# Kernel optimization log

Hardware: AMD Instinct MI355X
Metric: run time of the kernel (lower is better)

Reference implementation:

```python
import jax, jax.numpy as jnp
from jax import lax
import numpy as np

B, C, H, W = 4, 256, 64, 64
O, KH, KW = 256, 3, 3
STR, PAD, DIL = 1, 1, 1
K = KH * KW
EPS = 1e-5


def setup_inputs() -> dict:
    key = jax.random.key(0)
    ks = jax.random.split(key, 8)
    fan = 1.0 / np.sqrt(C * KH * KW)
    return {
        "input_x": jax.random.normal(ks[0], (B, C, H, W), jnp.float32),
        # offset-generating conv (DeformConv2dPack style): 2*K channels of (dy, dx)
        "w_offset": jax.random.normal(ks[1], (2 * K, C, KH, KW), jnp.float32) * 0.01,
        "b_offset": jnp.zeros((2 * K,), jnp.float32),
        # deformable conv weight / bias
        "weight": jax.random.normal(ks[2], (O, C, KH, KW), jnp.float32) * fan,
        "bias": jax.random.normal(ks[3], (O,), jnp.float32) * 0.01,
        # BatchNorm2d params + running stats (inference mode)
        "gamma": jax.random.normal(ks[4], (O,), jnp.float32) * 0.1 + 1.0,
        "beta": jax.random.normal(ks[5], (O,), jnp.float32) * 0.1,
        "run_mean": jax.random.normal(ks[6], (O,), jnp.float32) * 0.1,
        "run_var": jax.random.uniform(ks[7], (O,), jnp.float32, 0.5, 1.5),
    }


def _bilinear_sample(img, y, x):
    """img: [B,C,H,W]; y,x: [B,K,Ho,Wo] float sample coords. Zero outside."""
    y0 = jnp.floor(y)
    x0 = jnp.floor(x)
    ly = y - y0
    lx = x - x0
    y0i = y0.astype(jnp.int32)
    x0i = x0.astype(jnp.int32)
    y1i = y0i + 1
    x1i = x0i + 1

    def valid(yi, xi):
        return ((yi >= 0) & (yi < H) & (xi >= 0) & (xi < W)).astype(img.dtype)

    # per-corner interpolation weights, zeroed when the corner is out of bounds
    w00 = (1 - ly) * (1 - lx) * valid(y0i, x0i)
    w01 = (1 - ly) * lx * valid(y0i, x1i)
    w10 = ly * (1 - lx) * valid(y1i, x0i)
    w11 = ly * lx * valid(y1i, x1i)

    y0c = jnp.clip(y0i, 0, H - 1)
    y1c = jnp.clip(y1i, 0, H - 1)
    x0c = jnp.clip(x0i, 0, W - 1)
    x1c = jnp.clip(x1i, 0, W - 1)

    gather = jax.vmap(lambda im, yi, xi: im[:, yi, xi])  # -> [B,C,K,Ho,Wo]
    out = gather(img, y0c, x0c) * w00[:, None]
    out = out + gather(img, y0c, x1c) * w01[:, None]
    out = out + gather(img, y1c, x0c) * w10[:, None]
    out = out + gather(img, y1c, x1c) * w11[:, None]
    return out  # [B,C,K,Ho,Wo]


def reference(input_x, w_offset, b_offset, weight, bias, gamma, beta, run_mean, run_var):
    # 1) generate offsets with a regular conv (DeformConv2dPack conv_offset)
    offset = lax.conv_general_dilated(
        input_x, w_offset, (STR, STR), [(PAD, PAD), (PAD, PAD)],
        rhs_dilation=(DIL, DIL), dimension_numbers=("NCHW", "OIHW", "NCHW"))
    offset = offset + b_offset[None, :, None, None]  # [B, 2K, Ho, Wo]
    Ho, Wo = offset.shape[2], offset.shape[3]
    off = offset.reshape(B, K, 2, Ho, Wo)
    dy, dx = off[:, :, 0], off[:, :, 1]  # [B,K,Ho,Wo]

    # 2) base sampling grid for each kernel tap
    ky, kx = jnp.meshgrid(jnp.arange(KH), jnp.arange(KW), indexing="ij")
    base_y = (jnp.arange(Ho) * STR - PAD)[None, :, None] + (ky.reshape(-1) * DIL)[:, None, None]
    base_x = (jnp.arange(Wo) * STR - PAD)[None, None, :] + (kx.reshape(-1) * DIL)[:, None, None]
    y = base_y.astype(input_x.dtype) + dy  # [B,K,Ho,Wo]
    x = base_x.astype(input_x.dtype) + dx

    # 3) bilinear-sampled im2col then dense contraction
    sampled = _bilinear_sample(input_x, y, x)  # [B,C,K,Ho,Wo]
    out = jnp.einsum("bckhw,ock->bohw", sampled, weight.reshape(O, C, K))
    out = out + bias[None, :, None, None]

    # 4) BatchNorm (inference, running stats) + ReLU
    inv = gamma / jnp.sqrt(run_var + EPS)
    out = out * inv[None, :, None, None] + (beta - run_mean * inv)[None, :, None, None]
    return jax.nn.relu(out)
```

## Files before the change

kernel.cpp:

```cpp
#include <hip/hip_runtime.h>
#include <math.h>

typedef __attribute__((ext_vector_type(8))) short b8;
typedef __attribute__((ext_vector_type(4))) float f4;
typedef float f4u __attribute__((ext_vector_type(4), aligned(4)));
typedef _Float16 h8 __attribute__((ext_vector_type(8)));
typedef _Float16 h2 __attribute__((ext_vector_type(2)));

#define XT2   0
#define OF2   2097152
#define DW2   2392064
#define DP2   2981888
#define AF2   3571712
#define BF2   3866624
#define WH2   2392064
#define WL2   2428928

__device__ inline ushort f2bf(float f) {
  uint u = __float_as_uint(f);
  return (ushort)((u + 0x7FFFu + ((u >> 16) & 1u)) >> 16);
}
__device__ inline h2 u2h2(uint u) { union { uint u; h2 h; } x; x.u = u; return x.h; }
__device__ inline uint h22u(h2 h) { union { uint u; h2 h; } x; x.h = h; return x.u; }
__device__ inline uint duph(float f) {
  union { _Float16 h; ushort u; } x; x.h = (_Float16)f;
  return ((uint)x.u << 16) | x.u;
}

__global__ __launch_bounds__(256) void prep_k(
    const float* __restrict__ w, const float* __restrict__ wof,
    const float* __restrict__ bias,
    const float* __restrict__ gamma, const float* __restrict__ beta,
    const float* __restrict__ mean, const float* __restrict__ var,
    float* __restrict__ ws) {
  const int tid = blockIdx.x * 256 + threadIdx.x;
  const int l  = tid & 63;
  const int ot = (tid >> 6) & 15;
  const int f  = tid >> 10;
  const int o  = (ot << 4) + (l & 15);
  const float inv = gamma[o] * rsqrtf(var[o] + 1e-5f);
  {
    const int s  = f & 1;
    const int g  = f >> 1;
    const int cw = g / 9;
    const int kk = g - cw * 9;
    const int cb = (cw << 6) + (s << 5) + ((l >> 4) << 3);
    h8 pk;
#pragma unroll
    for (int j = 0; j < 8; ++j)
      pk[j] = (_Float16)(w[((o << 8) + cb + j) * 9 + kk] * inv);
    *(h8*)((_Float16*)(ws + AF2) + tid * 8) = pk;
    ((f4*)(ws + OF2))[tid] = f4{0.f, 0.f, 0.f, 0.f};
  }
  if (tid < 256) {
    const float iv = gamma[tid] * rsqrtf(var[tid] + 1e-5f);
    ws[BF2 + tid] = bias[tid] * iv + beta[tid] - mean[tid] * iv;
  }
  if (tid < 9216) {
    const int l2  = tid & 63;
    const int mt  = (tid >> 6) & 1;
    const int i2  = tid >> 7;
    const int cg2 = i2 / 9;
    const int kk2 = i2 - cg2 * 9;
    const int oc  = (mt << 4) + (l2 & 15);
    const int cb2 = (cg2 << 5) + ((l2 >> 4) << 3);
    b8 ph, pl;
#pragma unroll
    for (int j = 0; j < 8; ++j) {
      const float v = (oc < 18) ? wof[((oc << 8) + cb2 + j) * 9 + kk2] : 0.f;
      const ushort h = f2bf(v);
      const float hf = __uint_as_float((uint)h << 16);
      ph[j] = (short)h;
      pl[j] = (short)f2bf(v - hf);
    }
    *(b8*)((short*)(ws + WH2) + tid * 8) = ph;
    *(b8*)((short*)(ws + WL2) + tid * 8) = pl;
  }
}

__global__ __launch_bounds__(256) void transpose_k(
    const float* __restrict__ x, float* __restrict__ ws) {
  const int id  = blockIdx.x * 256 + threadIdx.x;
  const int p   = id & 4095;
  const int cg8 = (id >> 12) & 31;
  const int b   = id >> 17;
  const float* xp = x + (((long)(b * 256 + cg8 * 8)) << 12) + p;
  _Float16* xt = (_Float16*)(ws + XT2);
  h8 pk;
#pragma unroll
  for (int j = 0; j < 8; ++j) pk[j] = (_Float16)xp[(long)j << 12];
  *(h8*)(xt + ((((long)(b << 12) + p)) << 8) + (cg8 << 3)) = pk;
}

__global__ __launch_bounds__(256, 4) void offset_part_k(
    const float* __restrict__ x, float* __restrict__ ws) {
  __shared__ __align__(16) ushort Xh[3][66][40];
  __shared__ __align__(16) ushort Xl[3][66][40];
  const int bid = blockIdx.x;
  const int q   = bid >> 8;
  const int b   = (bid >> 6) & 3;
  const int ho  = bid & 63;
  const int t   = threadIdx.x;
  const int l   = t & 63;
  const int wv  = t >> 6;
  const short* afh = (const short*)(ws + WH2);
  const short* afl = (const short*)(ws + WL2);

  for (int u = t; u < 240; u += 256) {
    const int row = u / 80, rem = u % 80;
    const int col = (rem >= 40) ? 65 : 0;
    const int c   = rem % 40;
    Xh[row][col][c] = 0;
    Xl[row][col][c] = 0;
  }

  f4 acc[2];
  acc[0] = f4{0.f, 0.f, 0.f, 0.f};
  acc[1] = f4{0.f, 0.f, 0.f, 0.f};

  const int cidx = t >> 3;
  const int j8   = t & 7;
  const float* xc = x + ((long)b << 20) + ((long)cidx << 12);
  const int col = (wv << 4) + (l & 15);
  const int qc  = (l >> 4) << 3;

  for (int it = 0; it < 2; ++it) {
    const int cg = (q << 1) + it;
    __syncthreads();
    const float* xg = xc + ((long)(cg << 5) << 12);
#pragma unroll
    for (int rep = 0; rep < 6; ++rep) {
      const int fi   = (rep << 3) + j8;
      const int row  = fi >> 4;
      const int colf = (fi & 15) << 2;
      const int y = ho - 1 + row;
      f4u v = {0.f, 0.f, 0.f, 0.f};
      if (y >= 0 && y <= 63) v = *(const f4u*)(xg + (y << 6) + colf);
#pragma unroll
      for (int qq = 0; qq < 4; ++qq) {
        const ushort h = f2bf(v[qq]);
        const float hf = __uint_as_float((uint)h << 16);
        Xh[row][colf + 1 + qq][cidx] = h;
        Xl[row][colf + 1 + qq][cidx] = f2bf(v[qq] - hf);
      }
    }
    __syncthreads();
#pragma unroll
    for (int kk = 0; kk < 9; ++kk) {
      const int ky = kk / 3, kx = kk - ky * 3;
      const int i  = cg * 9 + kk;
      const b8 ah0 = *(const b8*)(afh + ((((i << 1) + 0) << 6) + l) * 8);
      const b8 ah1 = *(const b8*)(afh + ((((i << 1) + 1) << 6) + l) * 8);
      const b8 al0 = *(const b8*)(afl + ((((i << 1) + 0) << 6) + l) * 8);
      const b8 al1 = *(const b8*)(afl + ((((i << 1) + 1) << 6) + l) * 8);
      const b8 bh = *(const b8*)&Xh[ky][col + kx][qc];
      const b8 bl = *(const b8*)&Xl[ky][col + kx][qc];
      acc[0] = __builtin_amdgcn_mfma_f32_16x16x32_bf16(ah0, bh, acc[0], 0, 0, 0);
      acc[0] = __builtin_amdgcn_mfma_f32_16x16x32_bf16(ah0, bl, acc[0], 0, 0, 0);
      acc[0] = __builtin_amdgcn_mfma_f32_16x16x32_bf16(al0, bh, acc[0], 0, 0, 0);
      acc[1] = __builtin_amdgcn_mfma_f32_16x16x32_bf16(ah1, bh, acc[1], 0, 0, 0);
      acc[1] = __builtin_amdgcn_mfma_f32_16x16x32_bf16(ah1, bl, acc[1], 0, 0, 0);
      acc[1] = __builtin_amdgcn_mfma_f32_16x16x32_bf16(al1, bh, acc[1], 0, 0, 0);
    }
  }

  const int wo = col;
  const int q4 = (l >> 4) << 2;
#pragma unroll
  for (int mt = 0; mt < 2; ++mt)
#pragma unroll
    for (int r = 0; r < 4; ++r) {
      const int oc = (mt << 4) + q4 + r;
      if (oc < 18)
        atomicAdd(&ws[OF2 + ((b * 18 + oc) << 12) + (ho << 6) + wo],
                  acc[mt][r]);
    }
}

__global__ __launch_bounds__(256) void make_desc_xt(
    const float* __restrict__ bof, float* __restrict__ ws) {
  const int d  = blockIdx.x * 256 + threadIdx.x;
  const int k  = d >> 14;
  const int n  = d & 16383;
  const int b  = n >> 12;
  const int sp = n & 4095;
  const int ho = sp >> 6, wo = sp & 63;
  const int ky = k / 3, kx = k - ky * 3;
  const float dy = ws[OF2 + ((b * 18 + (k << 1)) << 12) + sp] + bof[k << 1];
  const float dx = ws[OF2 + ((b * 18 + (k << 1) + 1) << 12) + sp] + bof[(k << 1) + 1];
  const float py = (float)(ho - 1 + ky) + dy;
  const float px = (float)(wo - 1 + kx) + dx;
  const float y0f = floorf(py), x0f = floorf(px);
  const float ly = py - y0f, lx = px - x0f;
  const int y0 = (int)y0f, x0 = (int)x0f;
  const int y1 = y0 + 1, x1 = x0 + 1;
  const float vy0 = (y0 >= 0 && y0 < 64) ? 1.f : 0.f;
  const float vy1 = (y1 >= 0 && y1 < 64) ? 1.f : 0.f;
  const float vx0 = (x0 >= 0 && x0 < 64) ? 1.f : 0.f;
  const float vx1 = (x1 >= 0 && x1 < 64) ? 1.f : 0.f;
  const int y0c = min(max(y0, 0), 63), y1c = min(max(y1, 0), 63);
  const int x0c = min(max(x0, 0), 63), x1c = min(max(x1, 0), 63);
  uint4 wv;
  wv.x = duph((1.f - ly) * (1.f - lx) * vy0 * vx0);
  wv.y = duph((1.f - ly) * lx * vy0 * vx1);
  wv.z = duph(ly * (1.f - lx) * vy1 * vx0);
  wv.w = duph(ly * lx * vy1 * vx1);
  int4 pv;
  pv.x = (y0c << 6) + x0c;
  pv.y = (y0c << 6) + x1c;
  pv.z = (y1c << 6) + x0c;
  pv.w = (y1c << 6) + x1c;
  ((uint4*)(ws + DW2))[d] = wv;
  ((int4*)(ws + DP2))[d] = pv;
}

__global__ __launch_bounds__(256, 2) void deform_gemm_f16b(
    const float* __restrict__ ws, float* __restrict__ out) {
  __shared__ __align__(16) uint Bs[3][32][32];
  __shared__ uint4 dW[288];
  __shared__ int4  dP[288];

  const int t     = threadIdx.x;
  const int bid   = blockIdx.x;
  const int xcd   = bid & 7;
  const int batch = xcd >> 1;
  const int half  = xcd & 1;
  const int j     = bid >> 3;
  const int sp0   = (half << 11) + (j << 5);
  const int nd0   = (batch << 12) + sp0;
  const int l     = t & 63;
  const int wv    = t >> 6;

  const int sn  = ((wv & 1) << 4) | (l & 15);
  const int cg8 = ((wv >> 1) << 2) | (l >> 4);
  const uint* xtu = (const uint*)(ws + XT2) + ((long)batch << 19);
  const _Float16* af = (const _Float16*)(ws + AF2);

  for (int u = t; u < 288; u += 256) {
    const int kk = u >> 5, s = u & 31;
    const int dg = (kk << 14) + nd0 + s;
    dW[u] = ((const uint4*)(ws + DW2))[dg];
    dP[u] = ((const int4*)(ws + DP2))[dg];
  }
  __syncthreads();

  f4 acc[4][2];
#pragma unroll
  for (int m = 0; m < 4; ++m)
#pragma unroll
    for (int nt = 0; nt < 2; ++nt) acc[m][nt] = f4{0.f, 0.f, 0.f, 0.f};

  uint4 cset0[4], cset1[4];
  uint4 w0v, w1v, wq; int4 pq;
  h8 aA[4][2], aN[4][2];
  int kkd, kkg, cwg, bufc;

#define FRDD(W_, P_, KK_) do { const int u_ = ((KK_) << 5) + sn;             \
    W_ = dW[u_]; P_ = dP[u_]; } while (0)

#define FGATH(DST_, P_) do {                                                 \
    const int co_ = (cwg << 5) + (cg8 << 2);                                 \
    DST_[0] = *(const uint4*)(xtu + ((P_).x << 7) + co_);                    \
    DST_[1] = *(const uint4*)(xtu + ((P_).y << 7) + co_);                    \
    DST_[2] = *(const uint4*)(xtu + ((P_).z << 7) + co_);                    \
    DST_[3] = *(const uint4*)(xtu + ((P_).w << 7) + co_);                    \
  } while (0)

#define FCOMB(CS_, WV_, BUF_) do {                                           \
    const h2 wc0_ = u2h2((WV_).x), wc1_ = u2h2((WV_).y);                     \
    const h2 wc2_ = u2h2((WV_).z), wc3_ = u2h2((WV_).w);                     \
    uint4 r_;                                                                \
    r_.x = h22u(u2h2(CS_[0].x) * wc0_ + u2h2(CS_[1].x) * wc1_ +              \
                u2h2(CS_[2].x) * wc2_ + u2h2(CS_[3].x) * wc3_);              \
    r_.y = h22u(u2h2(CS_[0].y) * wc0_ + u2h2(CS_[1].y) * wc1_ +              \
                u2h2(CS_[2].y) * wc2_ + u2h2(CS_[3].y) * wc3_);              \
    r_.z = h22u(u2h2(CS_[0].z) * wc0_ + u2h2(CS_[1].z) * wc1_ +              \
                u2h2(CS_[2].z) * wc2_ + u2h2(CS_[3].z) * wc3_);              \
    r_.w = h22u(u2h2(CS_[0].w) * wc0_ + u2h2(CS_[1].w) * wc1_ +              \
                u2h2(CS_[2].w) * wc2_ + u2h2(CS_[3].w) * wc3_);              \
    *(uint4*)&Bs[BUF_][sn][(cg8 ^ (sn & 7)) << 2] = r_;                      \
  } while (0)

#define FLOADA(I_, DST_) do {                                                \
    _Pragma("unroll")                                                        \
    for (int m = 0; m < 4; ++m)                                              \
      _Pragma("unroll")                                                      \
      for (int s = 0; s < 2; ++s) {                                          \
        const int f_ = ((I_) << 1) + s;                                      \
        DST_[m][s] = *(const h8*)(af +                                       \
            ((((f_ << 4) + (wv << 2) + m) << 6) + l) * 8);                   \
      }                                                                      \
  } while (0)

#define FMFMA(AC_, BUF_) do {                                                \
    h8 bB_[2][2];                                                            \
    _Pragma("unroll")                                                        \
    for (int nt = 0; nt < 2; ++nt)                                           \
      _Pragma("unroll")                                                      \
      for (int s = 0; s < 2; ++s) {                                          \
        const int snr_ = (nt << 4) + (l & 15);                               \
        const int ph_  = (((s << 2) + (l >> 4)) ^ (snr_ & 7)) << 2;          \
        bB_[nt][s] = *(const h8*)&Bs[BUF_][snr_][ph_];                       \
      }                                                                      \
    _Pragma("unroll")                                                        \
    for (int m = 0; m < 4; ++m)                                              \
      _Pragma("unroll")                                                      \
      for (int nt = 0; nt < 2; ++nt) {                                       \
        acc[m][nt] = __builtin_amdgcn_mfma_f32_16x16x32_f16(                 \
            AC_[m][0], bB_[nt][0], acc[m][nt], 0, 0, 0);                     \
        acc[m][nt] = __builtin_amdgcn_mfma_f32_16x16x32_f16(                 \
            AC_[m][1], bB_[nt][1], acc[m][nt], 0, 0, 0);                     \
      }                                                                      \
  } while (0)

#define FBODY(I_, AC_, AN_, CC_, WC_, CN_, WN_) do {                         \
    if ((I_) < 34) {                                                         \
      WN_ = wq; FGATH(CN_, pq);                                              \
      kkg++; if (kkg == 9) { kkg = 0; cwg++; }                               \
    }                                                                        \
    if ((I_) < 33) { FRDD(wq, pq, kkd); kkd = (kkd == 8) ? 0 : kkd + 1; }    \
    const int bufn_ = (bufc == 2) ? 0 : bufc + 1;                            \
    FMFMA(AC_, bufc);                                                        \
    if ((I_) < 35) {                                                         \
      FLOADA((I_) + 1, AN_);                                                 \
      FCOMB(CC_, WC_, bufn_);                                                \
    }                                                                        \
    bufc = bufn_;                                                            \
    __syncthreads();                                                         \
  } while (0)

  {
    uint4 wA; int4 pA;
    cwg = 0;
    FRDD(wA, pA, 0);
    FGATH(cset0, pA);
    FRDD(w1v, pA, 1);
    FGATH(cset1, pA);
    FRDD(wq, pq, 2);
    FLOADA(0, aA);
    FCOMB(cset0, wA, 0);
    kkd = 3; kkg = 2; bufc = 0;
  }
  __syncthreads();

  for (int i = 0; i < 36; i += 2) {
    FBODY(i,     aA, aN, cset1, w1v, cset0, w0v);
    FBODY(i + 1, aN, aA, cset0, w0v, cset1, w1v);
  }

  const float* bfold = ws + BF2;
  const int quad = l >> 4;
  const int ow = wv << 6;
#pragma unroll
  for (int m = 0; m < 4; ++m) {
    const int ob = ow + (m << 4) + (quad << 2);
    const f4 bf = *(const f4*)&bfold[ob];
#pragma unroll
    for (int nt = 0; nt < 2; ++nt) {
      const int sp = sp0 + (nt << 4) + (l & 15);
#pragma unroll
      for (int r = 0; r < 4; ++r) {
        out[(((batch << 8) + ob + r) << 12) + sp] =
            fmaxf(acc[m][nt][r] + bf[r], 0.f);
      }
    }
  }
}

extern "C" void kernel_launch(void* const* d_in, const int* in_sizes, int n_in,
                              void* d_out, int out_size, void* d_ws, size_t ws_size,
                              hipStream_t stream) {
  const float* x     = (const float*)d_in[0];
  const float* wof   = (const float*)d_in[1];
  const float* bof   = (const float*)d_in[2];
  const float* w     = (const float*)d_in[3];
  const float* bias  = (const float*)d_in[4];
  const float* gamma = (const float*)d_in[5];
  const float* beta  = (const float*)d_in[6];
  const float* mean  = (const float*)d_in[7];
  const float* var   = (const float*)d_in[8];
  float* out = (float*)d_out;
  float* ws  = (float*)d_ws;

  hipLaunchKernelGGL(prep_k, dim3(288), dim3(256), 0, stream,
                     w, wof, bias, gamma, beta, mean, var, ws);
  hipLaunchKernelGGL(transpose_k, dim3(2048), dim3(256), 0, stream, x, ws);
  hipLaunchKernelGGL(offset_part_k, dim3(1024), dim3(256), 0, stream, x, ws);
  hipLaunchKernelGGL(make_desc_xt, dim3(576), dim3(256), 0, stream, bof, ws);
  hipLaunchKernelGGL(deform_gemm_f16b, dim3(512), dim3(256), 0, stream,
                     ws, out);
}
```

Baseline: 161.7 us.

## Merge prep and transpose kernels and compute sampling descriptors inside GEMM

The weight-prep and input-transpose kernels become a single launch, with the block index selecting which job each block does. The separate descriptor kernel is removed: the deformable GEMM now computes bilinear weights and corner indices directly from the offsets when it fills shared memory. This cuts two kernel launches and the global write and re-read of the descriptor buffers. In exchange, each GEMM block repeats the offset math in its prologue, which adds latency before the main loop.

```diff
diff --git a/kernel.cpp b/kernel.cpp
--- a/kernel.cpp
+++ b/kernel.cpp
@@ -9,12 +9,10 @@
 
 #define XT2   0
 #define OF2   2097152
-#define DW2   2392064
-#define DP2   2981888
+#define WH2   2392064
+#define WL2   2428928
 #define AF2   3571712
 #define BF2   3866624
-#define WH2   2392064
-#define WL2   2428928
 
 __device__ inline ushort f2bf(float f) {
   uint u = __float_as_uint(f);
@@ -27,13 +25,27 @@
   return ((uint)x.u << 16) | x.u;
 }
 
-__global__ __launch_bounds__(256) void prep_k(
-    const float* __restrict__ w, const float* __restrict__ wof,
-    const float* __restrict__ bias,
+__global__ __launch_bounds__(256) void pre_k(
+    const float* __restrict__ x, const float* __restrict__ w,
+    const float* __restrict__ wof, const float* __restrict__ bias,
     const float* __restrict__ gamma, const float* __restrict__ beta,
     const float* __restrict__ mean, const float* __restrict__ var,
     float* __restrict__ ws) {
-  const int tid = blockIdx.x * 256 + threadIdx.x;
+  const int bid = blockIdx.x;
+  if (bid < 2048) {
+    const int id  = bid * 256 + threadIdx.x;
+    const int p   = id & 4095;
+    const int cg8 = (id >> 12) & 31;
+    const int b   = id >> 17;
+    const float* xp = x + (((long)(b * 256 + cg8 * 8)) << 12) + p;
+    _Float16* xt = (_Float16*)(ws + XT2);
+    h8 pk;
+#pragma unroll
+    for (int j = 0; j < 8; ++j) pk[j] = (_Float16)xp[(long)j << 12];
+    *(h8*)(xt + ((((long)(b << 12) + p)) << 8) + (cg8 << 3)) = pk;
+    return;
+  }
+  const int tid = (bid - 2048) * 256 + threadIdx.x;
   const int l  = tid & 63;
   const int ot = (tid >> 6) & 15;
   const int f  = tid >> 10;
@@ -76,20 +88,6 @@
     *(b8*)((short*)(ws + WH2) + tid * 8) = ph;
     *(b8*)((short*)(ws + WL2) + tid * 8) = pl;
   }
-}
-
-__global__ __launch_bounds__(256) void transpose_k(
-    const float* __restrict__ x, float* __restrict__ ws) {
-  const int id  = blockIdx.x * 256 + threadIdx.x;
-  const int p   = id & 4095;
-  const int cg8 = (id >> 12) & 31;
-  const int b   = id >> 17;
-  const float* xp = x + (((long)(b * 256 + cg8 * 8)) << 12) + p;
-  _Float16* xt = (_Float16*)(ws + XT2);
-  h8 pk;
-#pragma unroll
-  for (int j = 0; j < 8; ++j) pk[j] = (_Float16)xp[(long)j << 12];
-  *(h8*)(xt + ((((long)(b << 12) + p)) << 8) + (cg8 << 3)) = pk;
 }
 
 __global__ __launch_bounds__(256, 4) void offset_part_k(
@@ -177,45 +175,9 @@
     }
 }
 
-__global__ __launch_bounds__(256) void make_desc_xt(
-    const float* __restrict__ bof, float* __restrict__ ws) {
-  const int d  = blockIdx.x * 256 + threadIdx.x;
-  const int k  = d >> 14;
-  const int n  = d & 16383;
-  const int b  = n >> 12;
-  const int sp = n & 4095;
-  const int ho = sp >> 6, wo = sp & 63;
-  const int ky = k / 3, kx = k - ky * 3;
-  const float dy = ws[OF2 + ((b * 18 + (k << 1)) << 12) + sp] + bof[k << 1];
-  const float dx = ws[OF2 + ((b * 18 + (k << 1) + 1) << 12) + sp] + bof[(k << 1) + 1];
-  const float py = (float)(ho - 1 + ky) + dy;
-  const float px = (float)(wo - 1 + kx) + dx;
-  const float y0f = floorf(py), x0f = floorf(px);
-  const float ly = py - y0f, lx = px - x0f;
-  const int y0 = (int)y0f, x0 = (int)x0f;
-  const int y1 = y0 + 1, x1 = x0 + 1;
-  const float vy0 = (y0 >= 0 && y0 < 64) ? 1.f : 0.f;
-  const float vy1 = (y1 >= 0 && y1 < 64) ? 1.f : 0.f;
-  const float vx0 = (x0 >= 0 && x0 < 64) ? 1.f : 0.f;
-  const float vx1 = (x1 >= 0 && x1 < 64) ? 1.f : 0.f;
-  const int y0c = min(max(y0, 0), 63), y1c = min(max(y1, 0), 63);
-  const int x0c = min(max(x0, 0), 63), x1c = min(max(x1, 0), 63);
-  uint4 wv;
-  wv.x = duph((1.f - ly) * (1.f - lx) * vy0 * vx0);
-  wv.y = duph((1.f - ly) * lx * vy0 * vx1);
-  wv.z = duph(ly * (1.f - lx) * vy1 * vx0);
-  wv.w = duph(ly * lx * vy1 * vx1);
-  int4 pv;
-  pv.x = (y0c << 6) + x0c;
-  pv.y = (y0c << 6) + x1c;
-  pv.z = (y1c << 6) + x0c;
-  pv.w = (y1c << 6) + x1c;
-  ((uint4*)(ws + DW2))[d] = wv;
-  ((int4*)(ws + DP2))[d] = pv;
-}
-
 __global__ __launch_bounds__(256, 2) void deform_gemm_f16b(
-    const float* __restrict__ ws, float* __restrict__ out) {
+    const float* __restrict__ ws, const float* __restrict__ bof,
+    float* __restrict__ out) {
   __shared__ __align__(16) uint Bs[3][32][32];
   __shared__ uint4 dW[288];
   __shared__ int4  dP[288];
@@ -227,7 +189,6 @@
   const int half  = xcd & 1;
   const int j     = bid >> 3;
   const int sp0   = (half << 11) + (j << 5);
-  const int nd0   = (batch << 12) + sp0;
   const int l     = t & 63;
   const int wv    = t >> 6;
 
@@ -238,9 +199,37 @@
 
   for (int u = t; u < 288; u += 256) {
     const int kk = u >> 5, s = u & 31;
-    const int dg = (kk << 14) + nd0 + s;
-    dW[u] = ((const uint4*)(ws + DW2))[dg];
-    dP[u] = ((const int4*)(ws + DP2))[dg];
+    const int sp = sp0 + s;
+    const int ho = sp >> 6, wo = sp & 63;
+    const int ky = kk / 3, kx = kk - ky * 3;
+    const float dy =
+        ws[OF2 + ((batch * 18 + (kk << 1)) << 12) + sp] + bof[kk << 1];
+    const float dx =
+        ws[OF2 + ((batch * 18 + (kk << 1) + 1) << 12) + sp] + bof[(kk << 1) + 1];
+    const float py = (float)(ho - 1 + ky) + dy;
+    const float px = (float)(wo - 1 + kx) + dx;
+    const float y0f = floorf(py), x0f = floorf(px);
+    const float ly = py - y0f, lx = px - x0f;
+    const int y0 = (int)y0f, x0 = (int)x0f;
+    const int y1 = y0 + 1, x1 = x0 + 1;
+    const float vy0 = (y0 >= 0 && y0 < 64) ? 1.f : 0.f;
+    const float vy1 = (y1 >= 0 && y1 < 64) ? 1.f : 0.f;
+    const float vx0 = (x0 >= 0 && x0 < 64) ? 1.f : 0.f;
+    const float vx1 = (x1 >= 0 && x1 < 64) ? 1.f : 0.f;
+    const int y0c = min(max(y0, 0), 63), y1c = min(max(y1, 0), 63);
+    const int x0c = min(max(x0, 0), 63), x1c = min(max(x1, 0), 63);
+    uint4 wv4;
+    wv4.x = duph((1.f - ly) * (1.f - lx) * vy0 * vx0);
+    wv4.y = duph((1.f - ly) * lx * vy0 * vx1);
+    wv4.z = duph(ly * (1.f - lx) * vy1 * vx0);
+    wv4.w = duph(ly * lx * vy1 * vx1);
+    int4 pv;
+    pv.x = (y0c << 6) + x0c;
+    pv.y = (y0c << 6) + x1c;
+    pv.z = (y1c << 6) + x0c;
+    pv.w = (y1c << 6) + x1c;
+    dW[u] = wv4;
+    dP[u] = pv;
   }
   __syncthreads();
 
@@ -382,11 +371,9 @@
   float* out = (float*)d_out;
   float* ws  = (float*)d_ws;
 
-  hipLaunchKernelGGL(prep_k, dim3(288), dim3(256), 0, stream,
-                     w, wof, bias, gamma, beta, mean, var, ws);
-  hipLaunchKernelGGL(transpose_k, dim3(2048), dim3(256), 0, stream, x, ws);
+  hipLaunchKernelGGL(pre_k, dim3(2336), dim3(256), 0, stream,
+                     x, w, wof, bias, gamma, beta, mean, var, ws);
   hipLaunchKernelGGL(offset_part_k, dim3(1024), dim3(256), 0, stream, x, ws);
-  hipLaunchKernelGGL(make_desc_xt, dim3(576), dim3(256), 0, stream, bof, ws);
   hipLaunchKernelGGL(deform_gemm_f16b, dim3(512), dim3(256), 0, stream,
-                     ws, out);
-}
+                     ws, bof, out);
+}
```

Measured after the change: 156.5 us. 3.2% less time.
